# Optimization experiments

Hardware: AMD Instinct MI355X
Metric: run time of the kernel (lower is better)

The kernel has to match this reference:

```python
import jax, jax.numpy as jnp
import numpy as np

B, N, C = 4, 2048, 768
H = 12
D = C // H  # head_dim = 64
SCALE = D ** -0.5


def setup_inputs() -> dict:
    key = jax.random.key(0)
    ks = jax.random.split(key, 9)
    x_q = jax.random.normal(ks[0], (B, N, C), dtype=jnp.float32)
    x_k = jax.random.normal(ks[1], (B, N, C), dtype=jnp.float32)
    x_v = jax.random.normal(ks[2], (B, N, C), dtype=jnp.float32)
    x_u = jax.random.uniform(ks[3], (B, N, C), dtype=jnp.float32)
    s = C ** -0.5
    Wq = jax.random.normal(ks[4], (C, C), dtype=jnp.float32) * s
    Wk = jax.random.normal(ks[5], (C, C), dtype=jnp.float32) * s
    Wv = jax.random.normal(ks[6], (C, C), dtype=jnp.float32) * s
    Wp = jax.random.normal(ks[7], (C, C), dtype=jnp.float32) * s
    bp = jax.random.normal(ks[8], (C,), dtype=jnp.float32) * 0.01
    return {"x_q": x_q, "x_k": x_k, "x_v": x_v, "x_u": x_u,
            "Wq": Wq, "Wk": Wk, "Wv": Wv, "Wp": Wp, "bp": bp}


def reference(x_q, x_k, x_v, x_u, Wq, Wk, Wv, Wp, bp):
    # Linear projections (torch Linear: y = x @ W.T), split into heads [B,H,N,D]
    def to_heads(x, W):
        y = jnp.einsum('bnc,oc->bno', x, W)
        return y.reshape(B, N, H, D).transpose(0, 2, 1, 3)
    q = to_heads(x_q, Wq) * SCALE
    k = to_heads(x_k, Wk)
    v = to_heads(x_v, Wv)
    # Scores [B,H,N,N]
    attn = jnp.einsum('bhqd,bhkd->bhqk', q, k)
    # Uncertainty map: per-query scalar (mean over channels), broadcast over keys & heads
    uc = jnp.mean(x_u, axis=-1)  # [B,N]
    attn = attn * uc[:, None, :, None]
    attn = jax.nn.softmax(attn, axis=-1)
    out = jnp.einsum('bhqk,bhkd->bhqd', attn, v)
    out = out.transpose(0, 2, 1, 3).reshape(B, N, C)
    return jnp.einsum('bnc,oc->bno', out, Wp) + bp
```

## Files before the change

kernel.cpp:

```cpp
#include <hip/hip_runtime.h>
#include <hip/hip_bf16.h>
#include <cstdint>

#define B_ 4
#define N_ 2048
#define C_ 768
#define H_ 12
#define D_ 64
#define QSCALE 0.18033688011112042f

typedef __bf16 bf16x8 __attribute__((ext_vector_type(8)));
typedef float f32x4 __attribute__((ext_vector_type(4)));
typedef float f32x16 __attribute__((ext_vector_type(16)));

__device__ __forceinline__ unsigned f2bs(float x) {
  unsigned u = __builtin_bit_cast(unsigned, x);
  unsigned r = (u + 0x7fffu + ((u >> 16) & 1u)) >> 16;
  return r;
}

__device__ __forceinline__ bf16x8 ldb8(const unsigned short* p) {
  return __builtin_bit_cast(bf16x8, *(const uint4*)p);
}

__device__ __forceinline__ f32x4 mfma16(bf16x8 a, bf16x8 b, f32x4 c) {
  return __builtin_amdgcn_mfma_f32_16x16x32_bf16(a, b, c, 0, 0, 0);
}

__device__ __forceinline__ f32x16 mfma32(bf16x8 a, bf16x8 b, f32x16 c) {
  return __builtin_amdgcn_mfma_f32_32x32x16_bf16(a, b, c, 0, 0, 0);
}

__device__ __forceinline__ void async16(const unsigned short* g, unsigned short* l) {
  __builtin_amdgcn_global_load_lds(
      (const __attribute__((address_space(1))) unsigned int*)g,
      (__attribute__((address_space(3))) unsigned int*)l, 16, 0, 0);
}

__global__ void prep_kernel(
    const float* __restrict__ xq, const float* __restrict__ xk,
    const float* __restrict__ xv, const float* __restrict__ xu,
    const float* __restrict__ Wq, const float* __restrict__ Wk,
    const float* __restrict__ Wv, const float* __restrict__ Wp,
    unsigned short* __restrict__ dxq, unsigned short* __restrict__ dxk,
    unsigned short* __restrict__ dxv,
    unsigned short* __restrict__ dwq, unsigned short* __restrict__ dwk,
    unsigned short* __restrict__ dwv, unsigned short* __restrict__ dwp,
    float* __restrict__ uc) {
  const int id = blockIdx.x;
  if (id < 18432) {
    const float* s = (id < 6144) ? xq : (id < 12288) ? xk : xv;
    unsigned short* d = (id < 6144) ? dxq : (id < 12288) ? dxk : dxv;
    int i = ((id % 6144) * 256 + threadIdx.x) * 4;
    float4 v = *(const float4*)(s + i);
    ushort4 h;
    h.x = (unsigned short)f2bs(v.x); h.y = (unsigned short)f2bs(v.y);
    h.z = (unsigned short)f2bs(v.z); h.w = (unsigned short)f2bs(v.w);
    *(ushort4*)(d + i) = h;
  } else if (id < 20736) {
    int sub = id - 18432;
    int which = sub / 576;
    const float* s = (which == 0) ? Wq : (which == 1) ? Wk : (which == 2) ? Wv : Wp;
    unsigned short* d = (which == 0) ? dwq : (which == 1) ? dwk : (which == 2) ? dwv : dwp;
    int i = ((sub % 576) * 256 + threadIdx.x) * 4;
    float4 v = *(const float4*)(s + i);
    ushort4 h;
    h.x = (unsigned short)f2bs(v.x); h.y = (unsigned short)f2bs(v.y);
    h.z = (unsigned short)f2bs(v.z); h.w = (unsigned short)f2bs(v.w);
    *(ushort4*)(d + i) = h;
  } else {
    int sub = id - 20736;
    int w = threadIdx.x >> 6, lane = threadIdx.x & 63;
    int row = sub * 4 + w;
    const float* p = xu + (size_t)row * C_;
    float s = 0.f;
#pragma unroll
    for (int i = 0; i < 3; ++i) {
      float4 v = *(const float4*)(p + (i * 64 + lane) * 4);
      s += v.x + v.y + v.z + v.w;
    }
#pragma unroll
    for (int off = 1; off < 64; off <<= 1) s += __shfl_xor(s, off);
    if (lane == 0) uc[row] = s * (1.f / 768.f);
  }
}

__device__ __forceinline__ void gemm_mainloop(
    const unsigned short* __restrict__ A, const unsigned short* __restrict__ W,
    int m0, int n0, unsigned short* Al, unsigned short* Bl,
    int tid, int wm, int wn, int quad, int id15, f32x4 (*acc)[4]) {
  const int wb = tid & 192;
  const unsigned short* ap[4];
  const unsigned short* bp[4];
#pragma unroll
  for (int s = 0; s < 4; ++s) {
    int g = s * 256 + tid;
    int row = (g >> 2) & 127;
    int col = ((g >> 9) << 5) | ((g & 3) << 3);
    ap[s] = A + (size_t)(m0 + row) * C_ + col;
    bp[s] = W + (size_t)(n0 + row) * C_ + col;
  }

  for (int kt = 0; kt < C_; kt += 64) {
    __syncthreads();
#pragma unroll
    for (int s = 0; s < 4; ++s) {
      async16(ap[s] + kt, Al + (s * 256 + wb) * 8);
      async16(bp[s] + kt, Bl + (s * 256 + wb) * 8);
    }
    __syncthreads();

#pragma unroll
    for (int kk = 0; kk < 2; ++kk) {
      bf16x8 af[4], bfr[4];
#pragma unroll
      for (int i = 0; i < 4; ++i)
        af[i]  = ldb8(&Al[kk * 4096 + (wm + i * 16 + id15) * 32 + quad * 8]);
#pragma unroll
      for (int j = 0; j < 4; ++j)
        bfr[j] = ldb8(&Bl[kk * 4096 + (wn + j * 16 + id15) * 32 + quad * 8]);
#pragma unroll
      for (int i = 0; i < 4; ++i)
#pragma unroll
        for (int j = 0; j < 4; ++j)
          acc[i][j] = mfma16(af[i], bfr[j], acc[i][j]);
    }
  }
}

#define TSTR 136
__global__ __launch_bounds__(256, 3) void gemm_qkv(
    const unsigned short* __restrict__ xq, const unsigned short* __restrict__ xk,
    const unsigned short* __restrict__ xv,
    const unsigned short* __restrict__ wq, const unsigned short* __restrict__ wk,
    const unsigned short* __restrict__ wv,
    unsigned short* __restrict__ oq, unsigned short* __restrict__ ok,
    unsigned short* __restrict__ ov, const float* __restrict__ uc) {
  __shared__ __align__(16) unsigned short S[128 * TSTR];
  unsigned short* Al = S;
  unsigned short* Bl = S + 8192;
  const int tid = threadIdx.x;
  const int w = tid >> 6, lane = tid & 63, quad = lane >> 4, id15 = lane & 15;
  const int wm = (w >> 1) << 6, wn = (w & 1) << 6;
  const int id = blockIdx.x;
  const int xcd = id & 7, slot = id >> 3;
  const int n0 = (slot % 6) << 7;
  const int gz = xcd * 24 + slot / 6;
  const int z = gz >> 6, m0 = (gz & 63) << 7;

  const unsigned short* A = (z == 0) ? xq : (z == 1) ? xk : xv;
  const unsigned short* W = (z == 0) ? wq : (z == 1) ? wk : wv;

  f32x4 acc[4][4] = {};
  gemm_mainloop(A, W, m0, n0, Al, Bl, tid, wm, wn, quad, id15, acc);

  if (z == 2) {
    __syncthreads();
#pragma unroll
    for (int i = 0; i < 4; ++i)
#pragma unroll
      for (int j = 0; j < 4; ++j) {
        uint2 u;
        u.x = f2bs(acc[i][j][0]) | (f2bs(acc[i][j][1]) << 16);
        u.y = f2bs(acc[i][j][2]) | (f2bs(acc[i][j][3]) << 16);
        *(uint2*)&S[(wn + j * 16 + id15) * TSTR + wm + i * 16 + quad * 4] = u;
      }
    __syncthreads();
    const int b = m0 >> 11, nb = m0 & (N_ - 1);
#pragma unroll
    for (int s = 0; s < 8; ++s) {
      int c = s * 256 + tid;
      int row = c >> 4, o = (c & 15) << 3;
      *(uint4*)(ov + (size_t)(b * C_ + n0 + row) * N_ + nb + o) = *(const uint4*)&S[row * TSTR + o];
    }
    return;
  }

#pragma unroll
  for (int i = 0; i < 4; ++i) {
#pragma unroll
    for (int j = 0; j < 4; ++j) {
#pragma unroll
      for (int r = 0; r < 4; ++r) {
        int gm = m0 + wm + i * 16 + quad * 4 + r;
        int gn = n0 + wn + j * 16 + id15;
        float v = acc[i][j][r];
        if (z == 0) {
          v *= QSCALE * uc[gm];
          oq[(size_t)gm * C_ + gn] = (unsigned short)f2bs(v);
        } else {
          ok[(size_t)gm * C_ + gn] = (unsigned short)f2bs(v);
        }
      }
    }
  }
}

__global__ __launch_bounds__(256, 4) void gemm_out(
    const unsigned short* __restrict__ ao, const unsigned short* __restrict__ wp,
    float* __restrict__ out, const float* __restrict__ bias) {
  __shared__ __align__(16) unsigned short Al[64 * 64];
  __shared__ __align__(16) unsigned short Bl[128 * 64];
  const int tid = threadIdx.x;
  const int w = tid >> 6, lane = tid & 63, quad = lane >> 4, id15 = lane & 15;
  const int wm = (w >> 1) << 5, wn = (w & 1) << 6;
  const int id = blockIdx.x;
  const int xcd = id & 7, slot = id >> 3;
  const int n0 = (slot % 6) << 7;
  const int m0 = (xcd * 16 + slot / 6) << 6;

  const int wb = tid & 192;
  const unsigned short* ap[2];
#pragma unroll
  for (int s = 0; s < 2; ++s) {
    int g = s * 256 + tid;
    int row = (g >> 2) & 63;
    int col = ((g >> 8) << 5) | ((g & 3) << 3);
    ap[s] = ao + (size_t)(m0 + row) * C_ + col;
  }
  const unsigned short* bp[4];
#pragma unroll
  for (int s = 0; s < 4; ++s) {
    int g = s * 256 + tid;
    int row = (g >> 2) & 127;
    int col = ((g >> 9) << 5) | ((g & 3) << 3);
    bp[s] = wp + (size_t)(n0 + row) * C_ + col;
  }

  f32x4 acc[2][4] = {};
  for (int kt = 0; kt < C_; kt += 64) {
    __syncthreads();
#pragma unroll
    for (int s = 0; s < 2; ++s) async16(ap[s] + kt, Al + (s * 256 + wb) * 8);
#pragma unroll
    for (int s = 0; s < 4; ++s) async16(bp[s] + kt, Bl + (s * 256 + wb) * 8);
    __syncthreads();

#pragma unroll
    for (int kk = 0; kk < 2; ++kk) {
      bf16x8 af[2], bfr[4];
#pragma unroll
      for (int i = 0; i < 2; ++i)
        af[i]  = ldb8(&Al[kk * 2048 + (wm + i * 16 + id15) * 32 + quad * 8]);
#pragma unroll
      for (int j = 0; j < 4; ++j)
        bfr[j] = ldb8(&Bl[kk * 4096 + (wn + j * 16 + id15) * 32 + quad * 8]);
#pragma unroll
      for (int i = 0; i < 2; ++i)
#pragma unroll
        for (int j = 0; j < 4; ++j)
          acc[i][j] = mfma16(af[i], bfr[j], acc[i][j]);
    }
  }

#pragma unroll
  for (int i = 0; i < 2; ++i) {
#pragma unroll
    for (int j = 0; j < 4; ++j) {
#pragma unroll
      for (int r = 0; r < 4; ++r) {
        int gm = m0 + wm + i * 16 + quad * 4 + r;
        int gn = n0 + wn + j * 16 + id15;
        out[(size_t)gm * C_ + gn] = acc[i][j][r] + bias[gn];
      }
    }
  }
}

#define KSTR 72
#define BUFO (64 * KSTR)
__global__ __launch_bounds__(256, 3) void attn_kernel(
    const unsigned short* __restrict__ Q, const unsigned short* __restrict__ Kk,
    const unsigned short* __restrict__ Vt, unsigned short* __restrict__ O) {
  __shared__ __align__(16) unsigned short Kl[2 * 64 * KSTR];

  const int tid = threadIdx.x;
  const int w = tid >> 6, lane = tid & 63;
  const int i32 = lane & 31, hi = lane >> 5;
  const int id = blockIdx.x;
  const int xcd = id & 7, slot = id >> 3;
  const int bh = xcd * 6 + (slot >> 4);
  const int qt = slot & 15;
  const int b = bh / H_, h = bh % H_;
  const int q0 = qt * 128 + w * 32;

  bf16x8 qf[4];
#pragma unroll
  for (int s = 0; s < 4; ++s)
    qf[s] = ldb8(Q + (size_t)(b * N_ + q0 + i32) * C_ + h * 64 + s * 16 + hi * 8);

  const uint4 onesu = {0x3F803F80u, 0x3F803F80u, 0x3F803F80u, 0x3F803F80u};
  const bf16x8 onesf = __builtin_bit_cast(bf16x8, onesu);

  f32x16 oacc0 = {}, oacc1 = {}, lacc = {};

  const size_t kbase = (size_t)(b * N_) * C_ + h * 64;
  const size_t vbase = (size_t)(b * C_ + h * 64) * N_;
  const int srow0 = tid >> 3, srow1 = 32 + (tid >> 3);
  const int sseg = (tid & 7) << 3;
  const unsigned short* vp = Vt + vbase + (size_t)i32 * N_ + hi * 8;

  {
    uint4 a0 = *(const uint4*)(Kk + kbase + (size_t)srow0 * C_ + sseg);
    uint4 a1 = *(const uint4*)(Kk + kbase + (size_t)srow1 * C_ + sseg);
    *(uint4*)&Kl[srow0 * KSTR + sseg] = a0;
    *(uint4*)&Kl[srow1 * KSTR + sseg] = a1;
  }

  int cur = 0;
  for (int kc = 0; kc < N_; kc += 64) {
    uint4 vr[4][2];
#pragma unroll
    for (int ks = 0; ks < 4; ++ks) {
      vr[ks][0] = *(const uint4*)(vp + kc + ks * 16);
      vr[ks][1] = *(const uint4*)(vp + 32 * N_ + kc + ks * 16);
    }
    const bool last = (kc + 64 >= N_);
    uint4 a0, a1;
    if (!last) {
      a0 = *(const uint4*)(Kk + kbase + (size_t)(kc + 64 + srow0) * C_ + sseg);
      a1 = *(const uint4*)(Kk + kbase + (size_t)(kc + 64 + srow1) * C_ + sseg);
    }

    asm volatile("s_waitcnt lgkmcnt(0)" ::: "memory");
    __builtin_amdgcn_s_barrier();

    const unsigned short* Kc = Kl + (cur ? BUFO : 0);
#pragma unroll
    for (int t = 0; t < 2; ++t) {
      f32x16 s16 = {};
#pragma unroll
      for (int s = 0; s < 4; ++s) {
        bf16x8 kf = ldb8(Kc + (t * 32 + i32) * KSTR + s * 16 + hi * 8);
        s16 = mfma32(kf, qf[s], s16);
      }
      unsigned Dw[8];
#pragma unroll
      for (int j = 0; j < 8; ++j) {
        float e0 = exp2f(s16[2 * j]);
        float e1 = exp2f(s16[2 * j + 1]);
        unsigned d;
        asm("v_cvt_pk_bf16_f32 %0, %1, %2" : "=v"(d) : "v"(e0), "v"(e1));
        Dw[j] = d;
      }
#pragma unroll
      for (int sl = 0; sl < 2; ++sl) {
        const int bb = sl * 4;
        unsigned x0 = Dw[bb + 0], y0 = Dw[bb + 2];
        unsigned x1 = Dw[bb + 1], y1 = Dw[bb + 3];
        asm("v_permlane32_swap_b32 %0, %1" : "+v"(x0), "+v"(y0));
        asm("v_permlane32_swap_b32 %0, %1" : "+v"(x1), "+v"(y1));
        uint4 u;
        u.x = x0;
        u.y = x1;
        u.z = y0;
        u.w = y1;
        bf16x8 pf = __builtin_bit_cast(bf16x8, u);
        lacc = mfma32(pf, onesf, lacc);
        oacc0 = mfma32(pf, __builtin_bit_cast(bf16x8, vr[2 * t + sl][0]), oacc0);
        oacc1 = mfma32(pf, __builtin_bit_cast(bf16x8, vr[2 * t + sl][1]), oacc1);
      }
    }

    if (!last) {
      unsigned short* Kn = Kl + (cur ? 0 : BUFO);
      *(uint4*)&Kn[srow0 * KSTR + sseg] = a0;
      *(uint4*)&Kn[srow1 * KSTR + sseg] = a1;
    }
    cur ^= 1;
  }

#pragma unroll
  for (int r = 0; r < 16; ++r) {
    float linv = 1.0f / lacc[r];
    int q = q0 + (r & 3) + 8 * (r >> 2) + 4 * hi;
    size_t base = (size_t)(b * N_ + q) * C_ + h * 64 + i32;
    O[base] = (unsigned short)f2bs(oacc0[r] * linv);
    O[base + 32] = (unsigned short)f2bs(oacc1[r] * linv);
  }
}

extern "C" void kernel_launch(void* const* d_in, const int* in_sizes, int n_in,
                              void* d_out, int out_size, void* d_ws, size_t ws_size,
                              hipStream_t stream) {
  const float* x_q = (const float*)d_in[0];
  const float* x_k = (const float*)d_in[1];
  const float* x_v = (const float*)d_in[2];
  const float* x_u = (const float*)d_in[3];
  const float* Wq  = (const float*)d_in[4];
  const float* Wk  = (const float*)d_in[5];
  const float* Wv  = (const float*)d_in[6];
  const float* Wp  = (const float*)d_in[7];
  const float* bp  = (const float*)d_in[8];

  char* ws = (char*)d_ws;
  size_t off = 0;
  auto alloc = [&](size_t bytes) {
    char* p = ws + off;
    off += (bytes + 255) & ~(size_t)255;
    return p;
  };
  unsigned short* wq16 = (unsigned short*)alloc((size_t)C_ * C_ * 2);
  unsigned short* wk16 = (unsigned short*)alloc((size_t)C_ * C_ * 2);
  unsigned short* wv16 = (unsigned short*)alloc((size_t)C_ * C_ * 2);
  unsigned short* wp16 = (unsigned short*)alloc((size_t)C_ * C_ * 2);
  float*          ucp  = (float*)alloc((size_t)B_ * N_ * 4);
  unsigned short* xq16 = (unsigned short*)alloc((size_t)B_ * N_ * C_ * 2);
  unsigned short* xk16 = (unsigned short*)alloc((size_t)B_ * N_ * C_ * 2);
  unsigned short* xv16 = (unsigned short*)alloc((size_t)B_ * N_ * C_ * 2);
  unsigned short* q_s  = (unsigned short*)alloc((size_t)B_ * N_ * C_ * 2);
  unsigned short* k_s  = (unsigned short*)alloc((size_t)B_ * N_ * C_ * 2);
  unsigned short* vT   = (unsigned short*)alloc((size_t)B_ * N_ * C_ * 2);
  unsigned short* ao   = (unsigned short*)alloc((size_t)B_ * N_ * C_ * 2);

  prep_kernel<<<dim3(22784), 256, 0, stream>>>(x_q, x_k, x_v, x_u, Wq, Wk, Wv, Wp,
                                               xq16, xk16, xv16,
                                               wq16, wk16, wv16, wp16, ucp);
  gemm_qkv<<<dim3(1152), 256, 0, stream>>>(xq16, xk16, xv16, wq16, wk16, wv16,
                                           q_s, k_s, vT, ucp);
  attn_kernel<<<dim3(768), 256, 0, stream>>>(q_s, k_s, vT, ao);
  gemm_out<<<dim3(768), 256, 0, stream>>>(ao, wp16, (float*)d_out, bp);
}
```

Before: 317.2 us.

## Stage V tiles through double-buffered LDS and add MFMA priority hints

The attention kernel previously had each wave load its own V fragments directly from global memory every iteration, so each of the four waves fetched the same V tile. V is now loaded cooperatively by the block into a double-buffered LDS region next to K and read back from LDS for the PV MFMAs, cutting redundant global traffic per block. The change also brackets the MFMA sections with s_setprio to favour matrix-issue waves. LDS use doubles (about 36KB per block), which may limit occupancy at the requested 3 blocks per CU, and it adds LDS reads and bank pressure.

```diff
diff --git a/kernel.cpp b/kernel.cpp
--- a/kernel.cpp
+++ b/kernel.cpp
@@ -268,11 +268,12 @@
 }
 
 #define KSTR 72
-#define BUFO (64 * KSTR)
+#define VOFF (64 * KSTR)
+#define BUFO (2 * 64 * KSTR)
 __global__ __launch_bounds__(256, 3) void attn_kernel(
     const unsigned short* __restrict__ Q, const unsigned short* __restrict__ Kk,
     const unsigned short* __restrict__ Vt, unsigned short* __restrict__ O) {
-  __shared__ __align__(16) unsigned short Kl[2 * 64 * KSTR];
+  __shared__ __align__(16) unsigned short KV[2 * 2 * 64 * KSTR];
 
   const int tid = threadIdx.x;
   const int w = tid >> 6, lane = tid & 63;
@@ -298,42 +299,45 @@
   const size_t vbase = (size_t)(b * C_ + h * 64) * N_;
   const int srow0 = tid >> 3, srow1 = 32 + (tid >> 3);
   const int sseg = (tid & 7) << 3;
-  const unsigned short* vp = Vt + vbase + (size_t)i32 * N_ + hi * 8;
 
   {
     uint4 a0 = *(const uint4*)(Kk + kbase + (size_t)srow0 * C_ + sseg);
     uint4 a1 = *(const uint4*)(Kk + kbase + (size_t)srow1 * C_ + sseg);
-    *(uint4*)&Kl[srow0 * KSTR + sseg] = a0;
-    *(uint4*)&Kl[srow1 * KSTR + sseg] = a1;
+    uint4 c0 = *(const uint4*)(Vt + vbase + (size_t)srow0 * N_ + sseg);
+    uint4 c1 = *(const uint4*)(Vt + vbase + (size_t)srow1 * N_ + sseg);
+    *(uint4*)&KV[srow0 * KSTR + sseg] = a0;
+    *(uint4*)&KV[srow1 * KSTR + sseg] = a1;
+    *(uint4*)&KV[VOFF + srow0 * KSTR + sseg] = c0;
+    *(uint4*)&KV[VOFF + srow1 * KSTR + sseg] = c1;
   }
 
   int cur = 0;
   for (int kc = 0; kc < N_; kc += 64) {
-    uint4 vr[4][2];
-#pragma unroll
-    for (int ks = 0; ks < 4; ++ks) {
-      vr[ks][0] = *(const uint4*)(vp + kc + ks * 16);
-      vr[ks][1] = *(const uint4*)(vp + 32 * N_ + kc + ks * 16);
-    }
     const bool last = (kc + 64 >= N_);
-    uint4 a0, a1;
+    uint4 a0, a1, c0, c1;
     if (!last) {
-      a0 = *(const uint4*)(Kk + kbase + (size_t)(kc + 64 + srow0) * C_ + sseg);
-      a1 = *(const uint4*)(Kk + kbase + (size_t)(kc + 64 + srow1) * C_ + sseg);
+      const int kcn = kc + 64;
+      a0 = *(const uint4*)(Kk + kbase + (size_t)(kcn + srow0) * C_ + sseg);
+      a1 = *(const uint4*)(Kk + kbase + (size_t)(kcn + srow1) * C_ + sseg);
+      c0 = *(const uint4*)(Vt + vbase + (size_t)srow0 * N_ + kcn + sseg);
+      c1 = *(const uint4*)(Vt + vbase + (size_t)srow1 * N_ + kcn + sseg);
     }
 
     asm volatile("s_waitcnt lgkmcnt(0)" ::: "memory");
     __builtin_amdgcn_s_barrier();
 
-    const unsigned short* Kc = Kl + (cur ? BUFO : 0);
+    const unsigned short* Kc = KV + (cur ? BUFO : 0);
+    const unsigned short* Vc = Kc + VOFF;
 #pragma unroll
     for (int t = 0; t < 2; ++t) {
       f32x16 s16 = {};
+      __builtin_amdgcn_s_setprio(1);
 #pragma unroll
       for (int s = 0; s < 4; ++s) {
         bf16x8 kf = ldb8(Kc + (t * 32 + i32) * KSTR + s * 16 + hi * 8);
         s16 = mfma32(kf, qf[s], s16);
       }
+      __builtin_amdgcn_s_setprio(0);
       unsigned Dw[8];
 #pragma unroll
       for (int j = 0; j < 8; ++j) {
@@ -343,6 +347,7 @@
         asm("v_cvt_pk_bf16_f32 %0, %1, %2" : "=v"(d) : "v"(e0), "v"(e1));
         Dw[j] = d;
       }
+      __builtin_amdgcn_s_setprio(1);
 #pragma unroll
       for (int sl = 0; sl < 2; ++sl) {
         const int bb = sl * 4;
@@ -357,15 +362,20 @@
         u.w = y1;
         bf16x8 pf = __builtin_bit_cast(bf16x8, u);
         lacc = mfma32(pf, onesf, lacc);
-        oacc0 = mfma32(pf, __builtin_bit_cast(bf16x8, vr[2 * t + sl][0]), oacc0);
-        oacc1 = mfma32(pf, __builtin_bit_cast(bf16x8, vr[2 * t + sl][1]), oacc1);
-      }
+        bf16x8 v0 = ldb8(Vc + i32 * KSTR + (2 * t + sl) * 16 + hi * 8);
+        bf16x8 v1 = ldb8(Vc + (32 + i32) * KSTR + (2 * t + sl) * 16 + hi * 8);
+        oacc0 = mfma32(pf, v0, oacc0);
+        oacc1 = mfma32(pf, v1, oacc1);
+      }
+      __builtin_amdgcn_s_setprio(0);
     }
 
     if (!last) {
-      unsigned short* Kn = Kl + (cur ? 0 : BUFO);
+      unsigned short* Kn = KV + (cur ? 0 : BUFO);
       *(uint4*)&Kn[srow0 * KSTR + sseg] = a0;
       *(uint4*)&Kn[srow1 * KSTR + sseg] = a1;
+      *(uint4*)&Kn[VOFF + srow0 * KSTR + sseg] = c0;
+      *(uint4*)&Kn[VOFF + srow1 * KSTR + sseg] = c1;
     }
     cur ^= 1;
   }
```

Measured after the change: 290.5 us. 1.09x faster.
